# Kernel optimization log

Hardware: AMD Instinct MI355X
Metric: run time of the kernel (lower is better)

## Reference

```python
import jax, jax.numpy as jnp
import numpy as np

KS = 7       # neighborhood kernel size (fixed in __init__)
HEADS = 8    # num_heads (fixed in __init__)
LN_EPS = 1e-5


def _nbr_idx(L, k):
    # NATTEN-style clamped window: window start shifts inward at borders (no padding)
    starts = jnp.clip(jnp.arange(L) - k // 2, 0, L - k)
    idx = starts[:, None] + jnp.arange(k)            # [L, k] absolute neighbor coords
    rel = idx - jnp.arange(L)[:, None] + (k - 1)     # [L, k] rel-pos-bias index in [0, 2k-2]
    return idx, rel


def _na2d(x, qkv_w, qkv_b, proj_w, proj_b, rpb):
    # x: [B, H, W, C]  -> neighborhood attention with clamped 7x7 windows
    B, H, W, C = x.shape
    hd = C // HEADS
    qkv = x @ qkv_w.T + qkv_b                        # [B,H,W,3C]
    q, k, v = jnp.split(qkv, 3, axis=-1)
    q = q.reshape(B, H, W, HEADS, hd) * (hd ** -0.5)
    k = k.reshape(B, H, W, HEADS, hd)
    v = v.reshape(B, H, W, HEADS, hd)
    ri, rri = _nbr_idx(H, KS)                        # [H,KS]
    ci, rci = _nbr_idx(W, KS)                        # [W,KS]
    # gather neighborhoods: [B,H,W,KS,KS,heads,hd]
    kn = k[:, ri[:, None, :, None], ci[None, :, None, :]]
    vn = v[:, ri[:, None, :, None], ci[None, :, None, :]]
    scores = jnp.einsum('bijhd,bijpqhd->bhijpq', q, kn)   # [B,heads,H,W,KS,KS]
    bias = rpb[:, rri[:, None, :, None], rci[None, :, None, :]]  # [heads,H,W,KS,KS]
    scores = scores + bias[None]
    attn = jax.nn.softmax(scores.reshape(B, HEADS, H, W, KS * KS), axis=-1)
    vn = vn.reshape(B, H, W, KS * KS, HEADS, hd)
    out = jnp.einsum('bhijp,bijphd->bijhd', attn, vn)      # [B,H,W,heads,hd]
    out = out.reshape(B, H, W, C)
    return out @ proj_w.T + proj_b


def _layernorm(x, g, b):
    mu = jnp.mean(x, axis=-1, keepdims=True)
    var = jnp.mean((x - mu) ** 2, axis=-1, keepdims=True)
    return (x - mu) * jax.lax.rsqrt(var + LN_EPS) * g + b


def setup_inputs() -> dict:
    key = jax.random.key(0)
    ks = jax.random.split(key, 4)
    B, T, H, W, C = 2, 8, 48, 48, 64
    return {
        'q': jax.random.normal(ks[0], (B, T, H, W, C), dtype=jnp.float32),
        'qkv_w': jax.random.normal(ks[1], (3 * C, C), dtype=jnp.float32) * 0.02,
        'qkv_b': jnp.zeros((3 * C,), jnp.float32),
        'proj_w': jax.random.normal(ks[2], (C, C), dtype=jnp.float32) * 0.02,
        'proj_b': jnp.zeros((C,), jnp.float32),
        'rpb': jax.random.normal(ks[3], (HEADS, 2 * KS - 1, 2 * KS - 1), dtype=jnp.float32) * 0.02,
        'ln_g': jnp.ones((C,), jnp.float32),
        'ln_b': jnp.zeros((C,), jnp.float32),
    }


def reference(q, qkv_w, qkv_b, proj_w, proj_b, rpb, ln_g, ln_b):
    B, T, H, W, C = q.shape
    x = q.reshape(B * T, H, W, C)                    # '(b t) h w c'
    x = _na2d(x, qkv_w, qkv_b, proj_w, proj_b, rpb)  # wPT path
    x = x.reshape(B, T, H, W, C)
    return _layernorm(x, ln_g, ln_b)                 # norm_q; wGC=False
```

## Files before the change

kernel.cpp:

```cpp
#include <hip/hip_runtime.h>
#include <hip/hip_bf16.h>

#define BT   16
#define IH   48
#define IW   48
#define CH   64
#define NH   8
#define HD   8
#define KS   7
#define NPIX (BT*IH*IW)
#define QKVC 192
#define LN_EPS 1e-5f
#define QSCALE 0.35355339059327373f

#define TSH  4
#define TSW  8
#define TP   (TSH*TSW)
#define AOS  72

typedef __bf16 bf16_t;
typedef bf16_t bf16x8 __attribute__((ext_vector_type(8)));
typedef float  f32x4  __attribute__((ext_vector_type(4)));
typedef float  f32x2  __attribute__((ext_vector_type(2)));

__device__ __forceinline__ float bflo(unsigned u) { union { unsigned i; float f; } v; v.i = u << 16; return v.f; }
__device__ __forceinline__ float bfhi(unsigned u) { union { unsigned i; float f; } v; v.i = u & 0xffff0000u; return v.f; }
__device__ __forceinline__ f32x2 unp2(unsigned u) { f32x2 r; r.x = bflo(u); r.y = bfhi(u); return r; }

__device__ __forceinline__ bf16x8 pack_bf16x8(float4 lo, float4 hi) {
    bf16x8 r;
    r[0] = (bf16_t)lo.x; r[1] = (bf16_t)lo.y; r[2] = (bf16_t)lo.z; r[3] = (bf16_t)lo.w;
    r[4] = (bf16_t)hi.x; r[5] = (bf16_t)hi.y; r[6] = (bf16_t)hi.z; r[7] = (bf16_t)hi.w;
    return r;
}

__global__ __launch_bounds__(256) void qkv_kernel(
        const float* __restrict__ x,
        const float* __restrict__ w,
        const float* __restrict__ b,
        __hip_bfloat16* __restrict__ qkv) {
    const int gw   = blockIdx.x * 4 + (threadIdx.x >> 6);
    const int ngrp = gw % 3;
    const int mg   = gw / 3;
    const int l  = threadIdx.x & 63;
    const int m  = l & 15;
    const int kg = l >> 4;

    const int ch_base = ngrp * 64 + m * 4;
    const float4 bias4 = *(const float4*)(b + ch_base);
    const float scale = (ngrp == 0) ? QSCALE : 1.f;

    bf16x8 wb0[4], wb1[4];
    #pragma unroll
    for (int t = 0; t < 4; ++t) {
        const float* wr_ = w + (size_t)(ch_base + t) * CH + kg * 8;
        wb0[t] = pack_bf16x8(*(const float4*)(wr_),      *(const float4*)(wr_ + 4));
        wb1[t] = pack_bf16x8(*(const float4*)(wr_ + 32), *(const float4*)(wr_ + 36));
    }

    #pragma unroll
    for (int mm = 0; mm < 2; ++mm) {
        const int mtile = mg * 2 + mm;
        const float* xr = x + (size_t)(mtile * 16 + m) * CH + kg * 8;
        const bf16x8 a0 = pack_bf16x8(*(const float4*)(xr),      *(const float4*)(xr + 4));
        const bf16x8 a1 = pack_bf16x8(*(const float4*)(xr + 32), *(const float4*)(xr + 36));

        float val[4][4];
        #pragma unroll
        for (int t = 0; t < 4; ++t) {
            f32x4 acc = {0.f, 0.f, 0.f, 0.f};
            acc = __builtin_amdgcn_mfma_f32_16x16x32_bf16(a0, wb0[t], acc, 0, 0, 0);
            acc = __builtin_amdgcn_mfma_f32_16x16x32_bf16(a1, wb1[t], acc, 0, 0, 0);
            const float bias = (t == 0) ? bias4.x : (t == 1) ? bias4.y : (t == 2) ? bias4.z : bias4.w;
            #pragma unroll
            for (int r = 0; r < 4; ++r) val[t][r] = (acc[r] + bias) * scale;
        }
        #pragma unroll
        for (int r = 0; r < 4; ++r) {
            const int pix = mtile * 16 + kg * 4 + r;
            union { ushort4 u; __hip_bfloat16 hh[4]; } pk;
            #pragma unroll
            for (int t = 0; t < 4; ++t) pk.hh[t] = __float2bfloat16(val[t][r]);
            *reinterpret_cast<ushort4*>(qkv + (size_t)pix * QKVC + ch_base) = pk.u;
        }
    }
}

__global__ __launch_bounds__(256, 4) void attn_proj_ln_kernel(
        const __hip_bfloat16* __restrict__ qkv,
        const float* __restrict__ rpb,
        const float* __restrict__ pw,
        const float* __restrict__ pb,
        const float* __restrict__ g,
        const float* __restrict__ beta,
        float* __restrict__ out) {
    __shared__ __align__(16) __hip_bfloat16 ao[TP * AOS];

    const int blk  = blockIdx.x;
    const int n    = blk & 15;
    const int tile = blk >> 4;
    const int i0   = (tile / 6) * TSH;
    const int j0   = (tile % 6) * TSW;
    const int tid  = threadIdx.x;
    const size_t img = (size_t)n * (IH * IW);

    {
        const int h  = tid & 7;
        const int pl = tid >> 3;
        const int i  = i0 + (pl >> 3);
        const int j  = j0 + (pl & 7);

        f32x2 qv[4];
        {
            const uint4 u = *reinterpret_cast<const uint4*>(
                qkv + (img + i * IW + j) * QKVC + h * HD);
            qv[0] = unp2(u.x); qv[1] = unp2(u.y); qv[2] = unp2(u.z); qv[3] = unp2(u.w);
        }

        int si = i - 3; si = si < 0 ? 0 : (si > IH - KS ? IH - KS : si);
        int sj = j - 3; sj = sj < 0 ? 0 : (sj > IW - KS ? IW - KS : sj);
        const float* rp = rpb + h * (2*KS-1) * (2*KS-1) + (sj - j + (KS - 1));

        float lrun = 0.f;
        f32x2 acc[4];
        #pragma unroll
        for (int d = 0; d < 4; ++d) acc[d] = (f32x2){0.f, 0.f};

        for (int p = 0; p < KS; ++p) {
            const int ki = si + p;
            const float* rprow = rp + (ki - i + (KS - 1)) * (2*KS-1);
            const __hip_bfloat16* row = qkv + (img + ki * IW + sj) * QKVC + CH + h * HD;

            uint4 kb[KS];
            float rb[KS];
            #pragma unroll
            for (int qq = 0; qq < KS; ++qq) {
                kb[qq] = *reinterpret_cast<const uint4*>(row + qq * QKVC);
                rb[qq] = rprow[qq];
            }
            float e[KS];
            #pragma unroll
            for (int qq = 0; qq < KS; ++qq) {
                f32x2 s2 = qv[0] * unp2(kb[qq].x);
                s2 += qv[1] * unp2(kb[qq].y);
                s2 += qv[2] * unp2(kb[qq].z);
                s2 += qv[3] * unp2(kb[qq].w);
                e[qq] = __expf(s2.x + s2.y + rb[qq]);
            }
            uint4 vb[KS];
            #pragma unroll
            for (int qq = 0; qq < KS; ++qq)
                vb[qq] = *reinterpret_cast<const uint4*>(row + qq * QKVC + CH);
            #pragma unroll
            for (int qq = 0; qq < KS; ++qq) {
                lrun += e[qq];
                acc[0] += e[qq] * unp2(vb[qq].x);
                acc[1] += e[qq] * unp2(vb[qq].y);
                acc[2] += e[qq] * unp2(vb[qq].z);
                acc[3] += e[qq] * unp2(vb[qq].w);
            }
        }
        const float inv = 1.f / lrun;
        union { uint4 u; __hip_bfloat16 hh[8]; } pk;
        #pragma unroll
        for (int d = 0; d < 4; ++d) {
            pk.hh[2*d]   = __float2bfloat16(acc[d].x * inv);
            pk.hh[2*d+1] = __float2bfloat16(acc[d].y * inv);
        }
        *reinterpret_cast<uint4*>(ao + pl * AOS + h * HD) = pk.u;
    }
    __syncthreads();

    const int wv = tid >> 6;
    if (wv < 2) {
        const int l  = tid & 63;
        const int m  = l & 15;
        const int kg = l >> 4;

        const __hip_bfloat16* ar = ao + (wv * 16 + m) * AOS + kg * 8;
        const bf16x8 a0 = *reinterpret_cast<const bf16x8*>(ar);
        const bf16x8 a1 = *reinterpret_cast<const bf16x8*>(ar + 32);

        const int ch_base = m * 4;
        const float4 bias4 = *(const float4*)(pb + ch_base);

        float val[4][4];
        #pragma unroll
        for (int t = 0; t < 4; ++t) {
            const float* wr_ = pw + (size_t)(ch_base + t) * CH + kg * 8;
            const bf16x8 b0 = pack_bf16x8(*(const float4*)(wr_),      *(const float4*)(wr_ + 4));
            const bf16x8 b1 = pack_bf16x8(*(const float4*)(wr_ + 32), *(const float4*)(wr_ + 36));
            f32x4 acc = {0.f, 0.f, 0.f, 0.f};
            acc = __builtin_amdgcn_mfma_f32_16x16x32_bf16(a0, b0, acc, 0, 0, 0);
            acc = __builtin_amdgcn_mfma_f32_16x16x32_bf16(a1, b1, acc, 0, 0, 0);
            const float bias = (t == 0) ? bias4.x : (t == 1) ? bias4.y : (t == 2) ? bias4.z : bias4.w;
            #pragma unroll
            for (int r = 0; r < 4; ++r) val[t][r] = acc[r] + bias;
        }

        float sm[4];
        #pragma unroll
        for (int r = 0; r < 4; ++r) sm[r] = val[0][r] + val[1][r] + val[2][r] + val[3][r];
        #pragma unroll
        for (int mask = 1; mask <= 8; mask <<= 1) {
            #pragma unroll
            for (int r = 0; r < 4; ++r) sm[r] += __shfl_xor(sm[r], mask, 64);
        }
        float mu[4];
        #pragma unroll
        for (int r = 0; r < 4; ++r) mu[r] = sm[r] * (1.f / 64.f);

        float qs[4];
        #pragma unroll
        for (int r = 0; r < 4; ++r) {
            float a = val[0][r] - mu[r], bq = val[1][r] - mu[r];
            float c = val[2][r] - mu[r], d = val[3][r] - mu[r];
            qs[r] = a * a + bq * bq + c * c + d * d;
        }
        #pragma unroll
        for (int mask = 1; mask <= 8; mask <<= 1) {
            #pragma unroll
            for (int r = 0; r < 4; ++r) qs[r] += __shfl_xor(qs[r], mask, 64);
        }
        float rs[4];
        #pragma unroll
        for (int r = 0; r < 4; ++r) rs[r] = rsqrtf(qs[r] * (1.f / 64.f) + LN_EPS);

        const float4 g4  = *(const float4*)(g + ch_base);
        const float4 be4 = *(const float4*)(beta + ch_base);
        #pragma unroll
        for (int r = 0; r < 4; ++r) {
            const int pl = wv * 16 + kg * 4 + r;
            const int gi = i0 + (pl >> 3), gj = j0 + (pl & 7);
            float4 o;
            o.x = (val[0][r] - mu[r]) * rs[r] * g4.x + be4.x;
            o.y = (val[1][r] - mu[r]) * rs[r] * g4.y + be4.y;
            o.z = (val[2][r] - mu[r]) * rs[r] * g4.z + be4.z;
            o.w = (val[3][r] - mu[r]) * rs[r] * g4.w + be4.w;
            *reinterpret_cast<float4*>(out + (img + gi * IW + gj) * CH + ch_base) = o;
        }
    }
}

extern "C" void kernel_launch(void* const* d_in, const int* in_sizes, int n_in,
                              void* d_out, int out_size, void* d_ws, size_t ws_size,
                              hipStream_t stream) {
    const float* x      = (const float*)d_in[0];
    const float* qkv_w  = (const float*)d_in[1];
    const float* qkv_b  = (const float*)d_in[2];
    const float* proj_w = (const float*)d_in[3];
    const float* proj_b = (const float*)d_in[4];
    const float* rpb    = (const float*)d_in[5];
    const float* ln_g   = (const float*)d_in[6];
    const float* ln_b   = (const float*)d_in[7];
    float* out = (float*)d_out;

    __hip_bfloat16* qkv = (__hip_bfloat16*)d_ws;

    qkv_kernel<<<864, 256, 0, stream>>>(x, qkv_w, qkv_b, qkv);
    attn_proj_ln_kernel<<<1152, 256, 0, stream>>>(qkv, rpb, proj_w, proj_b,
                                                  ln_g, ln_b, out);
}
```

Measured before the change: 115.8 us.

## Process two vertically adjacent query pixels per thread to share K/V row loads

Each thread now computes attention for two query pixels in consecutive rows, iterating over a union of up to 8 key rows so each loaded K/V row is reused by both queries. The block shrinks to 128 threads, and both waves now do the projection/LN stage instead of half idling. Relative-position bias is loaded as two vectorised float4 reads per row. This cuts global K/V traffic roughly in half per output, in exchange for more registers per thread, extra predicated exp work, and fewer threads per block.

```diff
diff --git a/kernel.cpp b/kernel.cpp
--- a/kernel.cpp
+++ b/kernel.cpp
@@ -27,6 +27,10 @@
 __device__ __forceinline__ float bfhi(unsigned u) { union { unsigned i; float f; } v; v.i = u & 0xffff0000u; return v.f; }
 __device__ __forceinline__ f32x2 unp2(unsigned u) { f32x2 r; r.x = bflo(u); r.y = bfhi(u); return r; }
 
+__device__ __forceinline__ float4 ldf4u(const float* p) {
+    float4 r; __builtin_memcpy(&r, p, 16); return r;
+}
+
 __device__ __forceinline__ bf16x8 pack_bf16x8(float4 lo, float4 hi) {
     bf16x8 r;
     r[0] = (bf16_t)lo.x; r[1] = (bf16_t)lo.y; r[2] = (bf16_t)lo.z; r[3] = (bf16_t)lo.w;
@@ -86,7 +90,7 @@
     }
 }
 
-__global__ __launch_bounds__(256, 4) void attn_proj_ln_kernel(
+__global__ __launch_bounds__(128) void attn_proj_ln_kernel(
         const __hip_bfloat16* __restrict__ qkv,
         const float* __restrict__ rpb,
         const float* __restrict__ pw,
@@ -106,73 +110,116 @@
 
     {
         const int h  = tid & 7;
-        const int pl = tid >> 3;
-        const int i  = i0 + (pl >> 3);
-        const int j  = j0 + (pl & 7);
-
-        f32x2 qv[4];
+        const int pr = tid >> 3;
+        const int pi = pr >> 3;
+        const int pj = pr & 7;
+        const int i  = i0 + pi * 2;
+        const int j  = j0 + pj;
+        const int pl0 = pi * 16 + pj;
+        const int pl1 = pl0 + 8;
+
+        f32x2 q0[4], q1[4];
         {
             const uint4 u = *reinterpret_cast<const uint4*>(
                 qkv + (img + i * IW + j) * QKVC + h * HD);
-            qv[0] = unp2(u.x); qv[1] = unp2(u.y); qv[2] = unp2(u.z); qv[3] = unp2(u.w);
-        }
-
-        int si = i - 3; si = si < 0 ? 0 : (si > IH - KS ? IH - KS : si);
-        int sj = j - 3; sj = sj < 0 ? 0 : (sj > IW - KS ? IW - KS : sj);
-        const float* rp = rpb + h * (2*KS-1) * (2*KS-1) + (sj - j + (KS - 1));
-
-        float lrun = 0.f;
-        f32x2 acc[4];
-        #pragma unroll
-        for (int d = 0; d < 4; ++d) acc[d] = (f32x2){0.f, 0.f};
-
-        for (int p = 0; p < KS; ++p) {
-            const int ki = si + p;
-            const float* rprow = rp + (ki - i + (KS - 1)) * (2*KS-1);
-            const __hip_bfloat16* row = qkv + (img + ki * IW + sj) * QKVC + CH + h * HD;
-
-            uint4 kb[KS];
-            float rb[KS];
+            q0[0] = unp2(u.x); q0[1] = unp2(u.y); q0[2] = unp2(u.z); q0[3] = unp2(u.w);
+            const uint4 v = *reinterpret_cast<const uint4*>(
+                qkv + (img + (i + 1) * IW + j) * QKVC + h * HD);
+            q1[0] = unp2(v.x); q1[1] = unp2(v.y); q1[2] = unp2(v.z); q1[3] = unp2(v.w);
+        }
+
+        int si0 = i - 3;     si0 = si0 < 0 ? 0 : (si0 > IH - KS ? IH - KS : si0);
+        int si1 = i - 2;     si1 = si1 < 0 ? 0 : (si1 > IH - KS ? IH - KS : si1);
+        int sj  = j - 3;     sj  = sj  < 0 ? 0 : (sj  > IW - KS ? IW - KS : sj);
+        const int off    = si1 - si0;
+        const int rbase0 = si0 - i + 6;
+        const float* rpc = rpb + h * (2*KS-1) * (2*KS-1) + (sj - j + (KS - 1));
+
+        float lr0 = 0.f, lr1 = 0.f;
+        f32x2 a0[4], a1[4];
+        #pragma unroll
+        for (int d = 0; d < 4; ++d) { a0[d] = (f32x2){0.f,0.f}; a1[d] = (f32x2){0.f,0.f}; }
+
+        for (int p = 0; p < 8; ++p) {
+            if (p == 7 && off == 0) break;
+            const bool d0 = (p < 7);
+            const bool d1 = (p > 0) || (off == 0);
+            const __hip_bfloat16* row =
+                qkv + (img + (si0 + p) * IW + sj) * QKVC + CH + h * HD;
+
+            uint4 kb[KS], vb[KS];
             #pragma unroll
             for (int qq = 0; qq < KS; ++qq) {
                 kb[qq] = *reinterpret_cast<const uint4*>(row + qq * QKVC);
-                rb[qq] = rprow[qq];
-            }
-            float e[KS];
+                vb[qq] = *reinterpret_cast<const uint4*>(row + qq * QKVC + CH);
+            }
+            float4 r0a = {0,0,0,0}, r0b = {0,0,0,0}, r1a = {0,0,0,0}, r1b = {0,0,0,0};
+            if (d0) {
+                const float* rr = rpc + (rbase0 + p) * (2*KS-1);
+                r0a = ldf4u(rr); r0b = ldf4u(rr + 3);
+            }
+            if (d1) {
+                const float* rr = rpc + (rbase0 - 1 + p) * (2*KS-1);
+                r1a = ldf4u(rr); r1b = ldf4u(rr + 3);
+            }
+
+            float s0[KS], s1[KS];
             #pragma unroll
             for (int qq = 0; qq < KS; ++qq) {
-                f32x2 s2 = qv[0] * unp2(kb[qq].x);
-                s2 += qv[1] * unp2(kb[qq].y);
-                s2 += qv[2] * unp2(kb[qq].z);
-                s2 += qv[3] * unp2(kb[qq].w);
-                e[qq] = __expf(s2.x + s2.y + rb[qq]);
-            }
-            uint4 vb[KS];
-            #pragma unroll
-            for (int qq = 0; qq < KS; ++qq)
-                vb[qq] = *reinterpret_cast<const uint4*>(row + qq * QKVC + CH);
+                const f32x2 k0 = unp2(kb[qq].x), k1 = unp2(kb[qq].y);
+                const f32x2 k2 = unp2(kb[qq].z), k3 = unp2(kb[qq].w);
+                f32x2 t0 = q0[0]*k0 + q0[1]*k1 + q0[2]*k2 + q0[3]*k3;
+                f32x2 t1 = q1[0]*k0 + q1[1]*k1 + q1[2]*k2 + q1[3]*k3;
+                s0[qq] = t0.x + t0.y;
+                s1[qq] = t1.x + t1.y;
+            }
+            float e0[KS], e1[KS];
+            #pragma unroll
+            for (int qq = 0; qq < KS; ++qq) { e0[qq] = 0.f; e1[qq] = 0.f; }
+            if (d0) {
+                e0[0] = __expf(s0[0] + r0a.x); e0[1] = __expf(s0[1] + r0a.y);
+                e0[2] = __expf(s0[2] + r0a.z); e0[3] = __expf(s0[3] + r0a.w);
+                e0[4] = __expf(s0[4] + r0b.y); e0[5] = __expf(s0[5] + r0b.z);
+                e0[6] = __expf(s0[6] + r0b.w);
+            }
+            if (d1) {
+                e1[0] = __expf(s1[0] + r1a.x); e1[1] = __expf(s1[1] + r1a.y);
+                e1[2] = __expf(s1[2] + r1a.z); e1[3] = __expf(s1[3] + r1a.w);
+                e1[4] = __expf(s1[4] + r1b.y); e1[5] = __expf(s1[5] + r1b.z);
+                e1[6] = __expf(s1[6] + r1b.w);
+            }
             #pragma unroll
             for (int qq = 0; qq < KS; ++qq) {
-                lrun += e[qq];
-                acc[0] += e[qq] * unp2(vb[qq].x);
-                acc[1] += e[qq] * unp2(vb[qq].y);
-                acc[2] += e[qq] * unp2(vb[qq].z);
-                acc[3] += e[qq] * unp2(vb[qq].w);
-            }
-        }
-        const float inv = 1.f / lrun;
+                const f32x2 v0 = unp2(vb[qq].x), v1 = unp2(vb[qq].y);
+                const f32x2 v2 = unp2(vb[qq].z), v3 = unp2(vb[qq].w);
+                lr0 += e0[qq];
+                a0[0] += e0[qq] * v0; a0[1] += e0[qq] * v1;
+                a0[2] += e0[qq] * v2; a0[3] += e0[qq] * v3;
+                lr1 += e1[qq];
+                a1[0] += e1[qq] * v0; a1[1] += e1[qq] * v1;
+                a1[2] += e1[qq] * v2; a1[3] += e1[qq] * v3;
+            }
+        }
+        const float inv0 = 1.f / lr0;
+        const float inv1 = 1.f / lr1;
         union { uint4 u; __hip_bfloat16 hh[8]; } pk;
         #pragma unroll
         for (int d = 0; d < 4; ++d) {
-            pk.hh[2*d]   = __float2bfloat16(acc[d].x * inv);
-            pk.hh[2*d+1] = __float2bfloat16(acc[d].y * inv);
-        }
-        *reinterpret_cast<uint4*>(ao + pl * AOS + h * HD) = pk.u;
+            pk.hh[2*d]   = __float2bfloat16(a0[d].x * inv0);
+            pk.hh[2*d+1] = __float2bfloat16(a0[d].y * inv0);
+        }
+        *reinterpret_cast<uint4*>(ao + pl0 * AOS + h * HD) = pk.u;
+        #pragma unroll
+        for (int d = 0; d < 4; ++d) {
+            pk.hh[2*d]   = __float2bfloat16(a1[d].x * inv1);
+            pk.hh[2*d+1] = __float2bfloat16(a1[d].y * inv1);
+        }
+        *reinterpret_cast<uint4*>(ao + pl1 * AOS + h * HD) = pk.u;
     }
     __syncthreads();
 
-    const int wv = tid >> 6;
-    if (wv < 2) {
+    {
+        const int wv = tid >> 6;
         const int l  = tid & 63;
         const int m  = l & 15;
         const int kg = l >> 4;
@@ -258,6 +305,6 @@
     __hip_bfloat16* qkv = (__hip_bfloat16*)d_ws;
 
     qkv_kernel<<<864, 256, 0, stream>>>(x, qkv_w, qkv_b, qkv);
-    attn_proj_ln_kernel<<<1152, 256, 0, stream>>>(qkv, rpb, proj_w, proj_b,
+    attn_proj_ln_kernel<<<1152, 128, 0, stream>>>(qkv, rpb, proj_w, proj_b,
                                                   ln_g, ln_b, out);
 }
```

Result: no change. 115.7 us (-0.1%).
